# Optimization experiments

Measured on AMD Instinct MI355X. Metric: run time of the kernel, lower is better.

## Reference

```python
import jax, jax.numpy as jnp
import numpy as np

EPS = 1e-5

def conv(x, w, b=None, groups=1):
    kh, kw = w.shape[2], w.shape[3]
    y = jax.lax.conv_general_dilated(
        x, w, (1, 1), ((kh // 2, kh // 2), (kw // 2, kw // 2)),
        dimension_numbers=('NCHW', 'OIHW', 'NCHW'), feature_group_count=groups)
    if b is not None:
        y = y + b[None, :, None, None]
    return y

def layernorm_c(x, g, b):
    # LayerNorm over channel dim (module permutes to NHWC, norms last dim, permutes back)
    mu = jnp.mean(x, axis=1, keepdims=True)
    var = jnp.mean(jnp.square(x - mu), axis=1, keepdims=True)
    return (x - mu) * jax.lax.rsqrt(var + EPS) * g[None, :, None, None] + b[None, :, None, None]

def _bilinear(img, py, px):
    # img: (N,C,H,W); py,px: (N,H,W) float sampling coords; zero outside bounds
    H, W = img.shape[2], img.shape[3]
    y0 = jnp.floor(py); x0 = jnp.floor(px)
    wy1 = py - y0; wy0 = 1.0 - wy1
    wx1 = px - x0; wx0 = 1.0 - wx1

    def gather(yc, xc):
        valid = (yc >= 0) & (yc <= H - 1) & (xc >= 0) & (xc <= W - 1)
        yi = jnp.clip(yc, 0, H - 1).astype(jnp.int32)
        xi = jnp.clip(xc, 0, W - 1).astype(jnp.int32)
        v = jax.vmap(lambda im, yy, xx: im[:, yy, xx])(img, yi, xi)  # (N,C,H,W)
        return v * valid[:, None].astype(img.dtype)

    return (gather(y0, x0) * (wy0 * wx0)[:, None]
            + gather(y0, x0 + 1) * (wy0 * wx1)[:, None]
            + gather(y0 + 1, x0) * (wy1 * wx0)[:, None]
            + gather(y0 + 1, x0 + 1) * (wy1 * wx1)[:, None])

def deform_conv2d(x, offset, weight, mask):
    # torchvision-style modulated deformable conv, 3x3, pad=1, stride=1
    N, C, H, W = x.shape
    by, bx = jnp.meshgrid(jnp.arange(H, dtype=x.dtype), jnp.arange(W, dtype=x.dtype), indexing='ij')
    out = jnp.zeros((N, weight.shape[0], H, W), dtype=x.dtype)
    for i in range(3):
        for j in range(3):
            k = i * 3 + j
            py = by[None] + (i - 1) + offset[:, 2 * k]      # (N,H,W)
            px = bx[None] + (j - 1) + offset[:, 2 * k + 1]
            samp = _bilinear(x, py, px) * mask[:, k][:, None]  # (N,C,H,W)
            out = out + jnp.einsum('nchw,oc->nohw', samp, weight[:, :, i, j])
    return out

def _forward(input_flow, input_event,
             ln_flow_g, ln_flow_b, ln_event_g, ln_event_b,
             ff_w1, ff_b1, ff_w2, ff_b2,
             fo_w1, fo_b1, fo_w2, fo_b2,
             fm_w1, fm_b1, fm_w2, fm_b2,
             dc_weight,
             sf_w1, sf_b1, sf_w2, sf_b2, sf_w3, sf_b3, sf_w4, sf_b4,
             fl_w1, fl_b1, fl_w2, fl_b2):
    N, C, H, W = input_flow.shape
    flow_norm = layernorm_c(input_flow, ln_flow_g, ln_flow_b)
    event_norm = layernorm_c(input_event, ln_event_g, ln_event_b)
    x = conv(jax.nn.relu(conv(flow_norm, ff_w1, ff_b1)), ff_w2, ff_b2, groups=C)
    offset = conv(jax.nn.relu(conv(event_norm, fo_w1, fo_b1)), fo_w2, fo_b2)
    mask = jax.nn.sigmoid(conv(jax.nn.relu(conv(event_norm, fm_w1, fm_b1)), fm_w2, fm_b2))
    dc = deform_conv2d(x, offset, dc_weight, mask)
    x_fft = jnp.fft.rfft2(x)            # (N,C,H,W//2+1) complex
    dc_fft = jnp.fft.rfft2(dc)
    fft_cate = jnp.concatenate([dc_fft.real, dc_fft.imag], axis=1)  # (N,2C,H,Wf)
    h = conv(fft_cate, sf_w1, sf_b1)
    h = conv(h, sf_w2, sf_b2, groups=2 * C)
    h = jax.nn.relu(conv(h, sf_w3, sf_b3))
    sp_mask = jax.nn.sigmoid(conv(h, sf_w4, sf_b4))  # (N,C,H,Wf) real
    x_irfft = jnp.fft.irfft2(x_fft * sp_mask, s=(H, W))
    g = conv(x_irfft, fl_w1, fl_b1, groups=C)
    a, b = jnp.split(g, 2, axis=1)
    g = a * jax.nn.gelu(b, approximate=False)
    return conv(g, fl_w2, fl_b2) + input_flow

def setup_inputs() -> dict:
    key = jax.random.key(0)
    N, C, H, W = 8, 32, 256, 256
    ks = iter(jax.random.split(key, 64))
    rn = lambda shp, s=0.05: jax.random.normal(next(ks), shp, dtype=jnp.float32) * s
    d = {
        'input_flow': jax.random.normal(next(ks), (N, C, H, W), dtype=jnp.float32),
        'input_event': jax.random.normal(next(ks), (N, C, H, W), dtype=jnp.float32),
        'ln_flow_g': 1.0 + rn((C,), 0.1), 'ln_flow_b': rn((C,), 0.1),
        'ln_event_g': 1.0 + rn((C,), 0.1), 'ln_event_b': rn((C,), 0.1),
        'ff_w1': rn((C, C, 1, 1)), 'ff_b1': rn((C,)),
        'ff_w2': rn((C, 1, 3, 3)), 'ff_b2': rn((C,)),
        'fo_w1': rn((C, C, 1, 1)), 'fo_b1': rn((C,)),
        'fo_w2': rn((18, C, 3, 3)), 'fo_b2': rn((18,)),
        'fm_w1': rn((C, C, 1, 1)), 'fm_b1': rn((C,)),
        'fm_w2': rn((9, C, 3, 3)), 'fm_b2': rn((9,)),
        'dc_weight': rn((C, C, 3, 3)),
        'sf_w1': rn((2 * C, 2 * C, 1, 1)), 'sf_b1': rn((2 * C,)),
        'sf_w2': rn((2 * C, 1, 3, 3)), 'sf_b2': rn((2 * C,)),
        'sf_w3': rn((2 * C, 2 * C, 1, 1)), 'sf_b3': rn((2 * C,)),
        'sf_w4': rn((C, 2 * C, 1, 1)), 'sf_b4': rn((C,)),
        'fl_w1': rn((C, 1, 3, 3)), 'fl_b1': rn((C,)),
        'fl_w2': rn((C, C // 2, 1, 1)), 'fl_b2': rn((C,)),
    }
    return d

def reference(input_flow, input_event,
              ln_flow_g, ln_flow_b, ln_event_g, ln_event_b,
              ff_w1, ff_b1, ff_w2, ff_b2,
              fo_w1, fo_b1, fo_w2, fo_b2,
              fm_w1, fm_b1, fm_w2, fm_b2,
              dc_weight,
              sf_w1, sf_b1, sf_w2, sf_b2, sf_w3, sf_b3, sf_w4, sf_b4,
              fl_w1, fl_b1, fl_w2, fl_b2):
    return _forward(input_flow, input_event,
                    ln_flow_g, ln_flow_b, ln_event_g, ln_event_b,
                    ff_w1, ff_b1, ff_w2, ff_b2,
                    fo_w1, fo_b1, fo_w2, fo_b2,
                    fm_w1, fm_b1, fm_w2, fm_b2,
                    dc_weight,
                    sf_w1, sf_b1, sf_w2, sf_b2, sf_w3, sf_b3, sf_w4, sf_b4,
                    fl_w1, fl_b1, fl_w2, fl_b2)
```

## Files before the change

### kernel.cpp

```cpp
#include <hip/hip_runtime.h>
#include <cmath>

constexpr int kN = 8;
constexpr int kC = 32;
constexpr int kH = 256;
constexpr int kW = 256;
constexpr int kHW = kH * kW;
constexpr int kWF = 129;
constexpr int kHWF = kH * kWF;
constexpr float kPI = 3.14159265358979323846f;

__device__ __forceinline__ float sigmoidf_(float x) { return 1.f / (1.f + expf(-x)); }

__device__ __forceinline__ int xcd_swizzle(int bid, int nblk)
{
    int chunk = nblk >> 3;
    return (bid & 7) * chunk + (bid >> 3);
}

template <bool TWO>
__global__ __launch_bounds__(256) void lnmv_kernel(
    const float* __restrict__ in,
    const float* __restrict__ lng, const float* __restrict__ lnb,
    const float* __restrict__ w1, const float* __restrict__ b1, float* __restrict__ out1,
    const float* __restrict__ w2, const float* __restrict__ b2, float* __restrict__ out2)
{
    __shared__ __align__(16) float wl1[1024];
    __shared__ __align__(16) float wl2[TWO ? 1024 : 4];
    __shared__ float bl1[32], bl2[32], gl[32], bbl[32];
    int tid = threadIdx.x;
    for (int e = tid; e < 1024; e += 256) {
        wl1[e] = w1[e];
        if (TWO) wl2[e] = w2[e];
    }
    if (tid < 32) {
        bl1[tid] = b1[tid]; gl[tid] = lng[tid]; bbl[tid] = lnb[tid];
        if (TWO) bl2[tid] = b2[tid];
    }
    __syncthreads();

    int p = blockIdx.x * 256 + tid;
    int n = p >> 16;
    int rem = p & 65535;
    const float* base = in + (size_t)n * kC * kHW + rem;

    float v[32];
    float mu = 0.f;
#pragma unroll
    for (int c = 0; c < 32; ++c) { v[c] = base[(size_t)c * kHW]; mu += v[c]; }
    mu *= 0.03125f;
    float var = 0.f;
#pragma unroll
    for (int c = 0; c < 32; ++c) { float d = v[c] - mu; var += d * d; }
    var *= 0.03125f;
    float rs = rsqrtf(var + 1e-5f);
#pragma unroll
    for (int c = 0; c < 32; ++c) v[c] = (v[c] - mu) * rs * gl[c] + bbl[c];

    {
        float* o = out1 + (size_t)n * kC * kHW + rem;
#pragma unroll
        for (int oc = 0; oc < 32; ++oc) {
            const float4* wr = reinterpret_cast<const float4*>(wl1 + oc * 32);
            float acc = bl1[oc];
#pragma unroll
            for (int q = 0; q < 8; ++q) {
                float4 wv = wr[q];
                acc += wv.x * v[4*q] + wv.y * v[4*q+1] + wv.z * v[4*q+2] + wv.w * v[4*q+3];
            }
            o[(size_t)oc * kHW] = fmaxf(acc, 0.f);
        }
    }
    if (TWO) {
        float* o = out2 + (size_t)n * kC * kHW + rem;
#pragma unroll
        for (int oc = 0; oc < 32; ++oc) {
            const float4* wr = reinterpret_cast<const float4*>(wl2 + oc * 32);
            float acc = bl2[oc];
#pragma unroll
            for (int q = 0; q < 8; ++q) {
                float4 wv = wr[q];
                acc += wv.x * v[4*q] + wv.y * v[4*q+1] + wv.z * v[4*q+2] + wv.w * v[4*q+3];
            }
            o[(size_t)oc * kHW] = fmaxf(acc, 0.f);
        }
    }
}

__global__ __launch_bounds__(256) void dw3x3_kernel(
    const float* __restrict__ in, const float* __restrict__ w,
    const float* __restrict__ bias, float* __restrict__ out,
    int CH, int Hd, int Wd, int total)
{
    int sw = xcd_swizzle(blockIdx.x, gridDim.x);
    int idx = sw * 256 + threadIdx.x;
    if (idx >= total) return;
    int wx = idx % Wd;
    int rest = idx / Wd;
    int hy = rest % Hd;
    int pl = rest / Hd;
    int ch = pl % CH;

    const float* ip = in + (size_t)pl * Hd * Wd;
    const float* wp = w + ch * 9;
    float acc = bias[ch];
#pragma unroll
    for (int dy = -1; dy <= 1; ++dy) {
        int yy = hy + dy;
        if (yy < 0 || yy >= Hd) continue;
        const float* rp = ip + (size_t)yy * Wd;
#pragma unroll
        for (int dx = -1; dx <= 1; ++dx) {
            int xx = wx + dx;
            if (xx < 0 || xx >= Wd) continue;
            acc += rp[xx] * wp[(dy + 1) * 3 + (dx + 1)];
        }
    }
    out[idx] = acc;
}

template <int COUT, int COUTP, int ACT>
__global__ __launch_bounds__(256) void conv3x3_kernel(
    const float* __restrict__ in, const float* __restrict__ wg,
    const float* __restrict__ bias, float* __restrict__ out)
{
    __shared__ __align__(16) float wl[288 * COUTP];
    __shared__ float bl[COUT];
    int tid = threadIdx.x;
    for (int e = tid; e < 288 * COUTP; e += 256) {
        int oc = e % COUTP;
        int t = e / COUTP;
        wl[e] = (oc < COUT) ? wg[(oc * 32 + (t / 9)) * 9 + (t % 9)] : 0.f;
    }
    if (tid < COUT) bl[tid] = bias[tid];
    __syncthreads();

    int sw = xcd_swizzle(blockIdx.x, gridDim.x);
    int row = sw * 4 + (tid >> 6);
    int lane = tid & 63;
    int n = row >> 8;
    int h = row & 255;

    float acc[4][COUTP];
#pragma unroll
    for (int px = 0; px < 4; ++px)
#pragma unroll
        for (int oc = 0; oc < COUTP; ++oc) acc[px][oc] = (oc < COUT) ? bl[oc] : 0.f;

    const float* ib = in + (size_t)n * 32 * kHW;
    for (int ic = 0; ic < 32; ++ic) {
        const float* ipl = ib + (size_t)ic * kHW;
#pragma unroll
        for (int ky = 0; ky < 3; ++ky) {
            int yy = h + ky - 1;
            if (yy < 0 || yy > 255) continue;
            const float* rp = ipl + (size_t)yy * 256;
#pragma unroll
            for (int kx = 0; kx < 3; ++kx) {
                float val[4];
#pragma unroll
                for (int px = 0; px < 4; ++px) {
                    int xx = lane + px * 64 + kx - 1;
                    val[px] = (xx >= 0 && xx < 256) ? rp[xx] : 0.f;
                }
                const float4* wr = reinterpret_cast<const float4*>(wl + (ic * 9 + ky * 3 + kx) * COUTP);
#pragma unroll
                for (int q = 0; q < COUTP / 4; ++q) {
                    float4 wv = wr[q];
#pragma unroll
                    for (int px = 0; px < 4; ++px) {
                        acc[px][4*q+0] += val[px] * wv.x;
                        acc[px][4*q+1] += val[px] * wv.y;
                        acc[px][4*q+2] += val[px] * wv.z;
                        acc[px][4*q+3] += val[px] * wv.w;
                    }
                }
            }
        }
    }

    float* ob = out + (size_t)n * COUT * kHW + (size_t)h * 256;
#pragma unroll
    for (int oc = 0; oc < COUT; ++oc) {
#pragma unroll
        for (int px = 0; px < 4; ++px) {
            float r = acc[px][oc];
            if (ACT == 2) r = sigmoidf_(r);
            ob[(size_t)oc * kHW + lane + px * 64] = r;
        }
    }
}

__global__ __launch_bounds__(256) void deform_kernel(
    const float* __restrict__ x, const float* __restrict__ off,
    const float* __restrict__ msk, const float* __restrict__ wt,
    float* __restrict__ out)
{
    __shared__ __align__(16) float wl[9 * 32 * 32];
    int tid = threadIdx.x;
    for (int e = tid; e < 9216; e += 256) {
        int o = e & 31;
        int t = e >> 5;
        int c = t & 31;
        int k = t >> 5;
        wl[e] = wt[((size_t)(o * 32 + c)) * 9 + k];
    }
    __syncthreads();

    int sw = xcd_swizzle(blockIdx.x, gridDim.x);
    int row = sw * 4 + (tid >> 6);
    int lane = tid & 63;
    int n = row >> 8;
    int h = row & 255;
    int pixbase = h * 256 + lane;

    const float* offb = off + (size_t)n * 18 * kHW + pixbase;
    const float* mskb = msk + (size_t)n * 9 * kHW + pixbase;
    const float* xb = x + (size_t)n * 32 * kHW;

    float acc[4][32];
#pragma unroll
    for (int px = 0; px < 4; ++px)
#pragma unroll
        for (int oc = 0; oc < 32; ++oc) acc[px][oc] = 0.f;

    for (int k = 0; k < 9; ++k) {
        int ki = k / 3 - 1, kj = k % 3 - 1;
        int i00[4], i01[4], i10[4], i11[4];
        float w00[4], w01[4], w10[4], w11[4];
#pragma unroll
        for (int px = 0; px < 4; ++px) {
            int wx = lane + px * 64;
            float oy = offb[(size_t)(2 * k) * kHW + px * 64];
            float ox = offb[(size_t)(2 * k + 1) * kHW + px * 64];
            float m = mskb[(size_t)k * kHW + px * 64];
            float py = (float)(h + ki) + oy;
            float pxx = (float)(wx + kj) + ox;
            float y0f = floorf(py), x0f = floorf(pxx);
            float fy = py - y0f, fx = pxx - x0f;
            float vy0 = (y0f >= 0.f && y0f <= 255.f) ? 1.f : 0.f;
            float vy1 = (y0f >= -1.f && y0f <= 254.f) ? 1.f : 0.f;
            float vx0 = (x0f >= 0.f && x0f <= 255.f) ? 1.f : 0.f;
            float vx1 = (x0f >= -1.f && x0f <= 254.f) ? 1.f : 0.f;
            int y0 = min(max((int)y0f, 0), 255);
            int y1 = min(max((int)y0f + 1, 0), 255);
            int x0 = min(max((int)x0f, 0), 255);
            int x1 = min(max((int)x0f + 1, 0), 255);
            i00[px] = y0 * 256 + x0; i01[px] = y0 * 256 + x1;
            i10[px] = y1 * 256 + x0; i11[px] = y1 * 256 + x1;
            w00[px] = (1.f - fy) * (1.f - fx) * m * vy0 * vx0;
            w01[px] = (1.f - fy) * fx * m * vy0 * vx1;
            w10[px] = fy * (1.f - fx) * m * vy1 * vx0;
            w11[px] = fy * fx * m * vy1 * vx1;
        }
        for (int c = 0; c < 32; ++c) {
            const float* xp = xb + (size_t)c * kHW;
            float s[4];
#pragma unroll
            for (int px = 0; px < 4; ++px) {
                s[px] = w00[px] * xp[i00[px]] + w01[px] * xp[i01[px]] +
                        w10[px] * xp[i10[px]] + w11[px] * xp[i11[px]];
            }
            const float4* wr = reinterpret_cast<const float4*>(wl + (size_t)(k * 32 + c) * 32);
#pragma unroll
            for (int q = 0; q < 8; ++q) {
                float4 wv = wr[q];
#pragma unroll
                for (int px = 0; px < 4; ++px) {
                    acc[px][4*q+0] += s[px] * wv.x;
                    acc[px][4*q+1] += s[px] * wv.y;
                    acc[px][4*q+2] += s[px] * wv.z;
                    acc[px][4*q+3] += s[px] * wv.w;
                }
            }
        }
    }

    float* ob = out + (size_t)n * 32 * kHW + pixbase;
#pragma unroll
    for (int oc = 0; oc < 32; ++oc)
#pragma unroll
        for (int px = 0; px < 4; ++px)
            ob[(size_t)oc * kHW + px * 64] = acc[px][oc];
}

__device__ __forceinline__ void fft256_stages(float2* A, float2* Bb, const float2* tw,
                                              int lane, float sgn)
{
    float2* src = A;
    float2* dst = Bb;
#pragma unroll
    for (int s = 0; s < 4; ++s) {
        int m = 1 << (2 * s);
        int r = lane & (m - 1);
        int mc = lane - r;
        __syncthreads();
        float2 x0 = src[lane];
        float2 x1 = src[lane + 128];
        float2 x2 = src[lane + 64];
        float2 x3 = src[lane + 192];
        float2 wa = tw[mc];
        float2 wb = tw[mc + 64];
        float2 wc = tw[2 * mc];
        float way = wa.y * sgn, wby = wb.y * sgn, wcy = wc.y * sgn;
        float e1x = x0.x + x1.x, e1y = x0.y + x1.y;
        float d1x = x0.x - x1.x, d1y = x0.y - x1.y;
        float o1x = wa.x * d1x - way * d1y, o1y = wa.x * d1y + way * d1x;
        float e2x = x2.x + x3.x, e2y = x2.y + x3.y;
        float d2x = x2.x - x3.x, d2y = x2.y - x3.y;
        float o2x = wb.x * d2x - wby * d2y, o2y = wb.x * d2y + wby * d2x;
        int base = r + 4 * mc;
        float2 y0; y0.x = e1x + e2x; y0.y = e1y + e2y;
        float ex = e1x - e2x, ey = e1y - e2y;
        float2 y2; y2.x = wc.x * ex - wcy * ey; y2.y = wc.x * ey + wcy * ex;
        float2 y1; y1.x = o1x + o2x; y1.y = o1y + o2y;
        float ox = o1x - o2x, oy = o1y - o2y;
        float2 y3; y3.x = wc.x * ox - wcy * oy; y3.y = wc.x * oy + wcy * ox;
        dst[base] = y0;
        dst[base + m] = y1;
        dst[base + 2 * m] = y2;
        dst[base + 3 * m] = y3;
        float2* t = src; src = dst; dst = t;
    }
    __syncthreads();
}

__device__ __forceinline__ void make_tw(float2* tw, int tid)
{
    if (tid < 128) {
        float ang = -kPI * (float)tid / 128.f;
        float2 w; w.x = cosf(ang); w.y = sinf(ang);
        tw[tid] = w;
    }
}

__global__ __launch_bounds__(256) void fft_rows_r2c(const float* __restrict__ in,
                                                    float2* __restrict__ out)
{
    __shared__ float2 A[4][256];
    __shared__ float2 Bb[4][256];
    __shared__ float2 tw[128];
    int tid = threadIdx.x;
    int sub = tid >> 6, lane = tid & 63;
    make_tw(tw, tid);
    size_t row = (size_t)blockIdx.x * 4 + sub;
    const float* rp = in + row * 256;
#pragma unroll
    for (int r = 0; r < 4; ++r) {
        int i = lane + 64 * r;
        float2 a; a.x = rp[i]; a.y = 0.f;
        A[sub][i] = a;
    }
    fft256_stages(A[sub], Bb[sub], tw, lane, 1.f);
    float2* op = out + row * kWF;
    op[lane] = A[sub][lane];
    op[lane + 64] = A[sub][lane + 64];
    if (lane == 0) op[128] = A[sub][128];
}

__global__ __launch_bounds__(256) void fft_cols_c2c(float2* __restrict__ buf)
{
    __shared__ float2 A[4][256];
    __shared__ float2 Bb[4][256];
    __shared__ float2 tw[128];
    int tid = threadIdx.x;
    int sub = tid >> 6, lane = tid & 63;
    make_tw(tw, tid);
    int b = xcd_swizzle(blockIdx.x, gridDim.x);
    int p = b / 33;
    int col0 = (b % 33) * 4;
    int ncols = (col0 + 4 <= kWF) ? 4 : (kWF - col0);
    float2* base = buf + (size_t)p * kHWF + col0;
    for (int e = tid; e < 1024; e += 256) {
        int cc = e & 3, hh = e >> 2;
        if (cc < ncols) A[cc][hh] = base[(size_t)hh * kWF + cc];
    }
    fft256_stages(A[sub], Bb[sub], tw, lane, 1.f);
    for (int e = tid; e < 1024; e += 256) {
        int cc = e & 3, hh = e >> 2;
        if (cc < ncols) base[(size_t)hh * kWF + cc] = A[cc][hh];
    }
}

__global__ __launch_bounds__(256) void ifft_cols_mask(const float2* __restrict__ xf,
                                                      const float* __restrict__ spm,
                                                      float2* __restrict__ out)
{
    __shared__ float2 A[4][256];
    __shared__ float2 Bb[4][256];
    __shared__ float2 tw[128];
    int tid = threadIdx.x;
    int sub = tid >> 6, lane = tid & 63;
    make_tw(tw, tid);
    int b = xcd_swizzle(blockIdx.x, gridDim.x);
    int p = b / 33;
    int col0 = (b % 33) * 4;
    int ncols = (col0 + 4 <= kWF) ? 4 : (kWF - col0);
    const float2* xb = xf + (size_t)p * kHWF + col0;
    const float* mb = spm + (size_t)p * kHWF + col0;
    for (int e = tid; e < 1024; e += 256) {
        int cc = e & 3, hh = e >> 2;
        if (cc < ncols) {
            float2 a = xb[(size_t)hh * kWF + cc];
            float m = mb[(size_t)hh * kWF + cc];
            a.x *= m; a.y *= m;
            A[cc][hh] = a;
        }
    }
    fft256_stages(A[sub], Bb[sub], tw, lane, -1.f);
    float2* ob = out + (size_t)p * kHWF + col0;
    for (int e = tid; e < 1024; e += 256) {
        int cc = e & 3, hh = e >> 2;
        if (cc < ncols) ob[(size_t)hh * kWF + cc] = A[cc][hh];
    }
}

__global__ __launch_bounds__(256) void ifft_rows_c2r(const float2* __restrict__ in,
                                                     float* __restrict__ out)
{
    __shared__ float2 A[4][256];
    __shared__ float2 Bb[4][256];
    __shared__ float2 tw[128];
    int tid = threadIdx.x;
    int sub = tid >> 6, lane = tid & 63;
    make_tw(tw, tid);
    size_t row = (size_t)blockIdx.x * 4 + sub;
    const float2* ip = in + row * kWF;
#pragma unroll
    for (int r = 0; r < 4; ++r) {
        int k = lane + 64 * r;
        if (k <= 128) {
            A[sub][k] = ip[k];
        } else {
            float2 c = ip[256 - k];
            c.y = -c.y;
            A[sub][k] = c;
        }
    }
    fft256_stages(A[sub], Bb[sub], tw, lane, -1.f);
    float* op = out + row * 256;
#pragma unroll
    for (int r = 0; r < 4; ++r) {
        int k = lane + 64 * r;
        op[k] = A[sub][k].x * (1.f / 65536.f);
    }
}

template <int CIN, int COUT, int ACT, bool CPLX>
__global__ __launch_bounds__(256) void conv1x1_kernel(
    const void* __restrict__ inv, const float* __restrict__ wg,
    const float* __restrict__ bias, float* __restrict__ out)
{
    constexpr int PL = kHWF;
    __shared__ __align__(16) float wl[COUT * CIN];
    __shared__ float bl[COUT];
    int tid = threadIdx.x;
    for (int e = tid; e < COUT * CIN; e += 256) wl[e] = wg[e];
    if (tid < COUT) bl[tid] = bias[tid];
    __syncthreads();

    int p0 = blockIdx.x * 512 + tid;
    int p1 = p0 + 256;
    int n0 = p0 / PL, r0 = p0 % PL;
    int n1 = p1 / PL, r1 = p1 % PL;

    float v0[CIN], v1[CIN];
    if (CPLX) {
        const float2* in2 = (const float2*)inv;
#pragma unroll
        for (int c = 0; c < 32; ++c) {
            float2 a = in2[(size_t)(n0 * 32 + c) * PL + r0];
            float2 b = in2[(size_t)(n1 * 32 + c) * PL + r1];
            v0[c] = a.x; v0[32 + c] = a.y;
            v1[c] = b.x; v1[32 + c] = b.y;
        }
    } else {
        const float* inf_ = (const float*)inv;
#pragma unroll
        for (int c = 0; c < CIN; ++c) {
            v0[c] = inf_[(size_t)(n0 * CIN + c) * PL + r0];
            v1[c] = inf_[(size_t)(n1 * CIN + c) * PL + r1];
        }
    }

#pragma unroll
    for (int oc = 0; oc < COUT; ++oc) {
        const float4* wr = reinterpret_cast<const float4*>(wl + oc * CIN);
        float a0 = bl[oc], a1 = bl[oc];
#pragma unroll
        for (int q = 0; q < CIN / 4; ++q) {
            float4 wv = wr[q];
            a0 += wv.x * v0[4*q] + wv.y * v0[4*q+1] + wv.z * v0[4*q+2] + wv.w * v0[4*q+3];
            a1 += wv.x * v1[4*q] + wv.y * v1[4*q+1] + wv.z * v1[4*q+2] + wv.w * v1[4*q+3];
        }
        if (ACT == 1) { a0 = fmaxf(a0, 0.f); a1 = fmaxf(a1, 0.f); }
        if (ACT == 2) { a0 = sigmoidf_(a0); a1 = sigmoidf_(a1); }
        out[(size_t)(n0 * COUT + oc) * PL + r0] = a0;
        out[(size_t)(n1 * COUT + oc) * PL + r1] = a1;
    }
}

__global__ __launch_bounds__(256) void conv1x1_chain_kernel(
    const float* __restrict__ in, const float* __restrict__ w3,
    const float* __restrict__ b3, const float* __restrict__ w4,
    const float* __restrict__ b4, float* __restrict__ out)
{
    constexpr int PL = kHWF;
    __shared__ __align__(16) float wl3[64 * 64];
    __shared__ __align__(16) float wl4[32 * 64];
    __shared__ float bl3[64], bl4[32];
    int tid = threadIdx.x;
    for (int e = tid; e < 4096; e += 256) wl3[e] = w3[e];
    for (int e = tid; e < 2048; e += 256) wl4[e] = w4[e];
    if (tid < 64) bl3[tid] = b3[tid];
    if (tid < 32) bl4[tid] = b4[tid];
    __syncthreads();

    int p0 = blockIdx.x * 512 + tid;
    int p1 = p0 + 256;
    int n0 = p0 / PL, r0 = p0 % PL;
    int n1 = p1 / PL, r1 = p1 % PL;

    float v0[64], v1[64];
#pragma unroll
    for (int c = 0; c < 64; ++c) {
        v0[c] = in[(size_t)(n0 * 64 + c) * PL + r0];
        v1[c] = in[(size_t)(n1 * 64 + c) * PL + r1];
    }

    float t0[64], t1[64];
#pragma unroll
    for (int oc = 0; oc < 64; ++oc) {
        const float4* wr = reinterpret_cast<const float4*>(wl3 + oc * 64);
        float a0 = bl3[oc], a1 = bl3[oc];
#pragma unroll
        for (int q = 0; q < 16; ++q) {
            float4 wv = wr[q];
            a0 += wv.x * v0[4*q] + wv.y * v0[4*q+1] + wv.z * v0[4*q+2] + wv.w * v0[4*q+3];
            a1 += wv.x * v1[4*q] + wv.y * v1[4*q+1] + wv.z * v1[4*q+2] + wv.w * v1[4*q+3];
        }
        t0[oc] = fmaxf(a0, 0.f); t1[oc] = fmaxf(a1, 0.f);
    }

#pragma unroll
    for (int oc = 0; oc < 32; ++oc) {
        const float4* wr = reinterpret_cast<const float4*>(wl4 + oc * 64);
        float a0 = bl4[oc], a1 = bl4[oc];
#pragma unroll
        for (int q = 0; q < 16; ++q) {
            float4 wv = wr[q];
            a0 += wv.x * t0[4*q] + wv.y * t0[4*q+1] + wv.z * t0[4*q+2] + wv.w * t0[4*q+3];
            a1 += wv.x * t1[4*q] + wv.y * t1[4*q+1] + wv.z * t1[4*q+2] + wv.w * t1[4*q+3];
        }
        out[(size_t)(n0 * 32 + oc) * PL + r0] = sigmoidf_(a0);
        out[(size_t)(n1 * 32 + oc) * PL + r1] = sigmoidf_(a1);
    }
}

__global__ __launch_bounds__(256) void final_kernel(
    const float* __restrict__ g, const float* __restrict__ flow,
    const float* __restrict__ wg, const float* __restrict__ bias,
    float* __restrict__ out)
{
    __shared__ __align__(16) float wl[32 * 16];
    __shared__ float bl[32];
    int tid = threadIdx.x;
    for (int e = tid; e < 512; e += 256) wl[e] = wg[e];
    if (tid < 32) bl[tid] = bias[tid];
    __syncthreads();

    int p = blockIdx.x * 256 + tid;
    int n = p >> 16;
    int rem = p & 65535;
    const float* gb = g + (size_t)n * 32 * kHW + rem;

    float v[16];
#pragma unroll
    for (int c = 0; c < 16; ++c) {
        float a = gb[(size_t)c * kHW];
        float b = gb[(size_t)(16 + c) * kHW];
        float ge = 0.5f * b * (1.f + erff(b * 0.70710678118654752f));
        v[c] = a * ge;
    }

    const float* fb = flow + (size_t)n * 32 * kHW + rem;
    float* ob = out + (size_t)n * 32 * kHW + rem;
#pragma unroll
    for (int oc = 0; oc < 32; ++oc) {
        const float4* wr = reinterpret_cast<const float4*>(wl + oc * 16);
        float acc = bl[oc];
#pragma unroll
        for (int q = 0; q < 4; ++q) {
            float4 wv = wr[q];
            acc += wv.x * v[4*q] + wv.y * v[4*q+1] + wv.z * v[4*q+2] + wv.w * v[4*q+3];
        }
        ob[(size_t)oc * kHW] = acc + fb[(size_t)oc * kHW];
    }
}

extern "C" void kernel_launch(void* const* d_in, const int* in_sizes, int n_in,
                              void* d_out, int out_size, void* d_ws, size_t ws_size,
                              hipStream_t stream)
{
    (void)in_sizes; (void)n_in; (void)out_size; (void)ws_size;

    const float* input_flow  = (const float*)d_in[0];
    const float* input_event = (const float*)d_in[1];
    const float* ln_flow_g   = (const float*)d_in[2];
    const float* ln_flow_b   = (const float*)d_in[3];
    const float* ln_event_g  = (const float*)d_in[4];
    const float* ln_event_b  = (const float*)d_in[5];
    const float* ff_w1 = (const float*)d_in[6];
    const float* ff_b1 = (const float*)d_in[7];
    const float* ff_w2 = (const float*)d_in[8];
    const float* ff_b2 = (const float*)d_in[9];
    const float* fo_w1 = (const float*)d_in[10];
    const float* fo_b1 = (const float*)d_in[11];
    const float* fo_w2 = (const float*)d_in[12];
    const float* fo_b2 = (const float*)d_in[13];
    const float* fm_w1 = (const float*)d_in[14];
    const float* fm_b1 = (const float*)d_in[15];
    const float* fm_w2 = (const float*)d_in[16];
    const float* fm_b2 = (const float*)d_in[17];
    const float* dc_weight = (const float*)d_in[18];
    const float* sf_w1 = (const float*)d_in[19];
    const float* sf_b1 = (const float*)d_in[20];
    const float* sf_w2 = (const float*)d_in[21];
    const float* sf_b2 = (const float*)d_in[22];
    const float* sf_w3 = (const float*)d_in[23];
    const float* sf_b3 = (const float*)d_in[24];
    const float* sf_w4 = (const float*)d_in[25];
    const float* sf_b4 = (const float*)d_in[26];
    const float* fl_w1 = (const float*)d_in[27];
    const float* fl_b1 = (const float*)d_in[28];
    const float* fl_w2 = (const float*)d_in[29];
    const float* fl_b2 = (const float*)d_in[30];
    float* out = (float*)d_out;

    const size_t S = (size_t)16908288;
    float* A = (float*)d_ws;
    float* B = A + S;
    float* Cs = B + S;
    float* X = out;

    lnmv_kernel<false><<<2048, 256, 0, stream>>>(input_flow, ln_flow_g, ln_flow_b,
                                                 ff_w1, ff_b1, A,
                                                 nullptr, nullptr, nullptr);
    lnmv_kernel<true><<<2048, 256, 0, stream>>>(input_event, ln_event_g, ln_event_b,
                                                fo_w1, fo_b1, B,
                                                fm_w1, fm_b1, Cs);
    dw3x3_kernel<<<65536, 256, 0, stream>>>(A, ff_w2, ff_b2, X, 32, 256, 256, 16777216);
    conv3x3_kernel<18, 20, 0><<<512, 256, 0, stream>>>(B, fo_w2, fo_b2, A);
    conv3x3_kernel<9, 12, 2><<<512, 256, 0, stream>>>(Cs, fm_w2, fm_b2, B);
    deform_kernel<<<512, 256, 0, stream>>>(X, A, B, dc_weight, Cs);
    fft_rows_r2c<<<16384, 256, 0, stream>>>(X, (float2*)A);
    fft_cols_c2c<<<8448, 256, 0, stream>>>((float2*)A);
    fft_rows_r2c<<<16384, 256, 0, stream>>>(Cs, (float2*)B);
    fft_cols_c2c<<<8448, 256, 0, stream>>>((float2*)B);
    conv1x1_kernel<64, 64, 0, true><<<516, 256, 0, stream>>>((const void*)B, sf_w1, sf_b1, Cs);
    dw3x3_kernel<<<66048, 256, 0, stream>>>(Cs, sf_w2, sf_b2, B, 64, 256, 129, 16908288);
    conv1x1_chain_kernel<<<516, 256, 0, stream>>>(B, sf_w3, sf_b3, sf_w4, sf_b4, Cs);
    ifft_cols_mask<<<8448, 256, 0, stream>>>((const float2*)A, Cs, (float2*)B);
    ifft_rows_c2r<<<16384, 256, 0, stream>>>((const float2*)B, Cs);
    dw3x3_kernel<<<65536, 256, 0, stream>>>(Cs, fl_w1, fl_b1, A, 32, 256, 256, 16777216);
    final_kernel<<<2048, 256, 0, stream>>>(A, input_flow, fl_w2, fl_b2, out);
}
```

Measured before the change: 1.500 ms.

## Halve per-thread work in deform and 1x1 convs, widen column FFT tiles

The deformable conv kernel now handles 2 pixels per thread instead of 4 and launches twice the blocks. The 1x1 conv and chain kernels drop from two pixels per thread to one. Both changes cut register pressure and raise occupancy. The column FFT and inverse-FFT-with-mask kernels now process 16 columns per block in a padded (stride 17) shared layout instead of 4, so global loads along rows are wider and more coalesced. The cost is fewer blocks per FFT launch and more shared memory per block.

```diff
diff --git a/kernel.cpp b/kernel.cpp
--- a/kernel.cpp
+++ b/kernel.cpp
@@ -208,32 +208,33 @@
     __syncthreads();
 
     int sw = xcd_swizzle(blockIdx.x, gridDim.x);
-    int row = sw * 4 + (tid >> 6);
-    int lane = tid & 63;
+    int halfid = tid >> 7;
+    int l = tid & 127;
+    int row = sw * 2 + halfid;
     int n = row >> 8;
     int h = row & 255;
-    int pixbase = h * 256 + lane;
+    int pixbase = h * 256 + l;
 
     const float* offb = off + (size_t)n * 18 * kHW + pixbase;
     const float* mskb = msk + (size_t)n * 9 * kHW + pixbase;
     const float* xb = x + (size_t)n * 32 * kHW;
 
-    float acc[4][32];
-#pragma unroll
-    for (int px = 0; px < 4; ++px)
+    float acc[2][32];
+#pragma unroll
+    for (int px = 0; px < 2; ++px)
 #pragma unroll
         for (int oc = 0; oc < 32; ++oc) acc[px][oc] = 0.f;
 
     for (int k = 0; k < 9; ++k) {
         int ki = k / 3 - 1, kj = k % 3 - 1;
-        int i00[4], i01[4], i10[4], i11[4];
-        float w00[4], w01[4], w10[4], w11[4];
-#pragma unroll
-        for (int px = 0; px < 4; ++px) {
-            int wx = lane + px * 64;
-            float oy = offb[(size_t)(2 * k) * kHW + px * 64];
-            float ox = offb[(size_t)(2 * k + 1) * kHW + px * 64];
-            float m = mskb[(size_t)k * kHW + px * 64];
+        int i00[2], i01[2], i10[2], i11[2];
+        float w00[2], w01[2], w10[2], w11[2];
+#pragma unroll
+        for (int px = 0; px < 2; ++px) {
+            int wx = l + px * 128;
+            float oy = offb[(size_t)(2 * k) * kHW + px * 128];
+            float ox = offb[(size_t)(2 * k + 1) * kHW + px * 128];
+            float m = mskb[(size_t)k * kHW + px * 128];
             float py = (float)(h + ki) + oy;
             float pxx = (float)(wx + kj) + ox;
             float y0f = floorf(py), x0f = floorf(pxx);
@@ -253,11 +254,12 @@
             w10[px] = fy * (1.f - fx) * m * vy1 * vx0;
             w11[px] = fy * fx * m * vy1 * vx1;
         }
+#pragma unroll 2
         for (int c = 0; c < 32; ++c) {
             const float* xp = xb + (size_t)c * kHW;
-            float s[4];
-#pragma unroll
-            for (int px = 0; px < 4; ++px) {
+            float s[2];
+#pragma unroll
+            for (int px = 0; px < 2; ++px) {
                 s[px] = w00[px] * xp[i00[px]] + w01[px] * xp[i01[px]] +
                         w10[px] * xp[i10[px]] + w11[px] * xp[i11[px]];
             }
@@ -266,7 +268,7 @@
             for (int q = 0; q < 8; ++q) {
                 float4 wv = wr[q];
 #pragma unroll
-                for (int px = 0; px < 4; ++px) {
+                for (int px = 0; px < 2; ++px) {
                     acc[px][4*q+0] += s[px] * wv.x;
                     acc[px][4*q+1] += s[px] * wv.y;
                     acc[px][4*q+2] += s[px] * wv.z;
@@ -280,8 +282,8 @@
 #pragma unroll
     for (int oc = 0; oc < 32; ++oc)
 #pragma unroll
-        for (int px = 0; px < 4; ++px)
-            ob[(size_t)oc * kHW + px * 64] = acc[px][oc];
+        for (int px = 0; px < 2; ++px)
+            ob[(size_t)oc * kHW + px * 128] = acc[px][oc];
 }
 
 __device__ __forceinline__ void fft256_stages(float2* A, float2* Bb, const float2* tw,
@@ -325,6 +327,51 @@
     __syncthreads();
 }
 
+__device__ __forceinline__ void fft256_stages16(float2* A, float2* Bb, const float2* tw,
+                                                int t, int c, float sgn)
+{
+    float2* src = A;
+    float2* dst = Bb;
+#pragma unroll
+    for (int s = 0; s < 4; ++s) {
+        int m = 1 << (2 * s);
+        __syncthreads();
+#pragma unroll
+        for (int b = 0; b < 4; ++b) {
+            int q = t + (b << 4);
+            int r = q & (m - 1);
+            int mc = q - r;
+            float2 x0 = src[q * 17 + c];
+            float2 x1 = src[(q + 128) * 17 + c];
+            float2 x2 = src[(q + 64) * 17 + c];
+            float2 x3 = src[(q + 192) * 17 + c];
+            float2 wa = tw[mc];
+            float2 wb = tw[mc + 64];
+            float2 wc = tw[2 * mc];
+            float way = wa.y * sgn, wby = wb.y * sgn, wcy = wc.y * sgn;
+            float e1x = x0.x + x1.x, e1y = x0.y + x1.y;
+            float d1x = x0.x - x1.x, d1y = x0.y - x1.y;
+            float o1x = wa.x * d1x - way * d1y, o1y = wa.x * d1y + way * d1x;
+            float e2x = x2.x + x3.x, e2y = x2.y + x3.y;
+            float d2x = x2.x - x3.x, d2y = x2.y - x3.y;
+            float o2x = wb.x * d2x - wby * d2y, o2y = wb.x * d2y + wby * d2x;
+            int base = r + 4 * mc;
+            float2 y0; y0.x = e1x + e2x; y0.y = e1y + e2y;
+            float ex = e1x - e2x, ey = e1y - e2y;
+            float2 y2; y2.x = wc.x * ex - wcy * ey; y2.y = wc.x * ey + wcy * ex;
+            float2 y1; y1.x = o1x + o2x; y1.y = o1y + o2y;
+            float ox = o1x - o2x, oy = o1y - o2y;
+            float2 y3; y3.x = wc.x * ox - wcy * oy; y3.y = wc.x * oy + wcy * ox;
+            dst[base * 17 + c] = y0;
+            dst[(base + m) * 17 + c] = y1;
+            dst[(base + 2 * m) * 17 + c] = y2;
+            dst[(base + 3 * m) * 17 + c] = y3;
+        }
+        float2* tp = src; src = dst; dst = tp;
+    }
+    __syncthreads();
+}
+
 __device__ __forceinline__ void make_tw(float2* tw, int tid)
 {
     if (tid < 128) {
@@ -358,60 +405,62 @@
     if (lane == 0) op[128] = A[sub][128];
 }
 
-__global__ __launch_bounds__(256) void fft_cols_c2c(float2* __restrict__ buf)
-{
-    __shared__ float2 A[4][256];
-    __shared__ float2 Bb[4][256];
+__global__ __launch_bounds__(256) void fft_cols16(float2* __restrict__ buf)
+{
+    __shared__ float2 A[256 * 17];
+    __shared__ float2 Bb[256 * 17];
     __shared__ float2 tw[128];
     int tid = threadIdx.x;
-    int sub = tid >> 6, lane = tid & 63;
     make_tw(tw, tid);
     int b = xcd_swizzle(blockIdx.x, gridDim.x);
-    int p = b / 33;
-    int col0 = (b % 33) * 4;
-    int ncols = (col0 + 4 <= kWF) ? 4 : (kWF - col0);
+    int p = b / 9;
+    int grp = b % 9;
+    int col0 = grp * 16;
+    int ncols = (col0 + 16 <= kWF) ? 16 : (kWF - col0);
     float2* base = buf + (size_t)p * kHWF + col0;
-    for (int e = tid; e < 1024; e += 256) {
-        int cc = e & 3, hh = e >> 2;
-        if (cc < ncols) A[cc][hh] = base[(size_t)hh * kWF + cc];
-    }
-    fft256_stages(A[sub], Bb[sub], tw, lane, 1.f);
-    for (int e = tid; e < 1024; e += 256) {
-        int cc = e & 3, hh = e >> 2;
-        if (cc < ncols) base[(size_t)hh * kWF + cc] = A[cc][hh];
-    }
-}
-
-__global__ __launch_bounds__(256) void ifft_cols_mask(const float2* __restrict__ xf,
-                                                      const float* __restrict__ spm,
-                                                      float2* __restrict__ out)
-{
-    __shared__ float2 A[4][256];
-    __shared__ float2 Bb[4][256];
+    for (int e = tid; e < 4096; e += 256) {
+        int pp = e >> 4, cc = e & 15;
+        if (cc < ncols) A[pp * 17 + cc] = base[(size_t)pp * kWF + cc];
+    }
+    int c = tid & 15, t = tid >> 4;
+    fft256_stages16(A, Bb, tw, t, c, 1.f);
+    for (int e = tid; e < 4096; e += 256) {
+        int pp = e >> 4, cc = e & 15;
+        if (cc < ncols) base[(size_t)pp * kWF + cc] = A[pp * 17 + cc];
+    }
+}
+
+__global__ __launch_bounds__(256) void ifft_cols_mask16(const float2* __restrict__ xf,
+                                                        const float* __restrict__ spm,
+                                                        float2* __restrict__ out)
+{
+    __shared__ float2 A[256 * 17];
+    __shared__ float2 Bb[256 * 17];
     __shared__ float2 tw[128];
     int tid = threadIdx.x;
-    int sub = tid >> 6, lane = tid & 63;
     make_tw(tw, tid);
     int b = xcd_swizzle(blockIdx.x, gridDim.x);
-    int p = b / 33;
-    int col0 = (b % 33) * 4;
-    int ncols = (col0 + 4 <= kWF) ? 4 : (kWF - col0);
+    int p = b / 9;
+    int grp = b % 9;
+    int col0 = grp * 16;
+    int ncols = (col0 + 16 <= kWF) ? 16 : (kWF - col0);
     const float2* xb = xf + (size_t)p * kHWF + col0;
     const float* mb = spm + (size_t)p * kHWF + col0;
-    for (int e = tid; e < 1024; e += 256) {
-        int cc = e & 3, hh = e >> 2;
+    for (int e = tid; e < 4096; e += 256) {
+        int pp = e >> 4, cc = e & 15;
         if (cc < ncols) {
-            float2 a = xb[(size_t)hh * kWF + cc];
-            float m = mb[(size_t)hh * kWF + cc];
+            float2 a = xb[(size_t)pp * kWF + cc];
+            float m = mb[(size_t)pp * kWF + cc];
             a.x *= m; a.y *= m;
-            A[cc][hh] = a;
-        }
-    }
-    fft256_stages(A[sub], Bb[sub], tw, lane, -1.f);
+            A[pp * 17 + cc] = a;
+        }
+    }
+    int c = tid & 15, t = tid >> 4;
+    fft256_stages16(A, Bb, tw, t, c, -1.f);
     float2* ob = out + (size_t)p * kHWF + col0;
-    for (int e = tid; e < 1024; e += 256) {
-        int cc = e & 3, hh = e >> 2;
-        if (cc < ncols) ob[(size_t)hh * kWF + cc] = A[cc][hh];
+    for (int e = tid; e < 4096; e += 256) {
+        int pp = e >> 4, cc = e & 15;
+        if (cc < ncols) ob[(size_t)pp * kWF + cc] = A[pp * 17 + cc];
     }
 }
 
@@ -459,44 +508,37 @@
     if (tid < COUT) bl[tid] = bias[tid];
     __syncthreads();
 
-    int p0 = blockIdx.x * 512 + tid;
-    int p1 = p0 + 256;
+    int p0 = blockIdx.x * 256 + tid;
     int n0 = p0 / PL, r0 = p0 % PL;
-    int n1 = p1 / PL, r1 = p1 % PL;
-
-    float v0[CIN], v1[CIN];
+
+    float v0[CIN];
     if (CPLX) {
         const float2* in2 = (const float2*)inv;
 #pragma unroll
         for (int c = 0; c < 32; ++c) {
             float2 a = in2[(size_t)(n0 * 32 + c) * PL + r0];
-            float2 b = in2[(size_t)(n1 * 32 + c) * PL + r1];
             v0[c] = a.x; v0[32 + c] = a.y;
-            v1[c] = b.x; v1[32 + c] = b.y;
         }
     } else {
         const float* inf_ = (const float*)inv;
 #pragma unroll
         for (int c = 0; c < CIN; ++c) {
             v0[c] = inf_[(size_t)(n0 * CIN + c) * PL + r0];
-            v1[c] = inf_[(size_t)(n1 * CIN + c) * PL + r1];
         }
     }
 
 #pragma unroll
     for (int oc = 0; oc < COUT; ++oc) {
         const float4* wr = reinterpret_cast<const float4*>(wl + oc * CIN);
-        float a0 = bl[oc], a1 = bl[oc];
+        float a0 = bl[oc];
 #pragma unroll
         for (int q = 0; q < CIN / 4; ++q) {
             float4 wv = wr[q];
             a0 += wv.x * v0[4*q] + wv.y * v0[4*q+1] + wv.z * v0[4*q+2] + wv.w * v0[4*q+3];
-            a1 += wv.x * v1[4*q] + wv.y * v1[4*q+1] + wv.z * v1[4*q+2] + wv.w * v1[4*q+3];
-        }
-        if (ACT == 1) { a0 = fmaxf(a0, 0.f); a1 = fmaxf(a1, 0.f); }
-        if (ACT == 2) { a0 = sigmoidf_(a0); a1 = sigmoidf_(a1); }
+        }
+        if (ACT == 1) a0 = fmaxf(a0, 0.f);
+        if (ACT == 2) a0 = sigmoidf_(a0);
         out[(size_t)(n0 * COUT + oc) * PL + r0] = a0;
-        out[(size_t)(n1 * COUT + oc) * PL + r1] = a1;
     }
 }
 
@@ -516,44 +558,36 @@
     if (tid < 32) bl4[tid] = b4[tid];
     __syncthreads();
 
-    int p0 = blockIdx.x * 512 + tid;
-    int p1 = p0 + 256;
+    int p0 = blockIdx.x * 256 + tid;
     int n0 = p0 / PL, r0 = p0 % PL;
-    int n1 = p1 / PL, r1 = p1 % PL;
-
-    float v0[64], v1[64];
-#pragma unroll
-    for (int c = 0; c < 64; ++c) {
-        v0[c] = in[(size_t)(n0 * 64 + c) * PL + r0];
-        v1[c] = in[(size_t)(n1 * 64 + c) * PL + r1];
-    }
-
-    float t0[64], t1[64];
+
+    float v0[64];
+#pragma unroll
+    for (int c = 0; c < 64; ++c) v0[c] = in[(size_t)(n0 * 64 + c) * PL + r0];
+
+    float t0[64];
 #pragma unroll
     for (int oc = 0; oc < 64; ++oc) {
         const float4* wr = reinterpret_cast<const float4*>(wl3 + oc * 64);
-        float a0 = bl3[oc], a1 = bl3[oc];
+        float a0 = bl3[oc];
 #pragma unroll
         for (int q = 0; q < 16; ++q) {
             float4 wv = wr[q];
             a0 += wv.x * v0[4*q] + wv.y * v0[4*q+1] + wv.z * v0[4*q+2] + wv.w * v0[4*q+3];
-            a1 += wv.x * v1[4*q] + wv.y * v1[4*q+1] + wv.z * v1[4*q+2] + wv.w * v1[4*q+3];
-        }
-        t0[oc] = fmaxf(a0, 0.f); t1[oc] = fmaxf(a1, 0.f);
+        }
+        t0[oc] = fmaxf(a0, 0.f);
     }
 
 #pragma unroll
     for (int oc = 0; oc < 32; ++oc) {
         const float4* wr = reinterpret_cast<const float4*>(wl4 + oc * 64);
-        float a0 = bl4[oc], a1 = bl4[oc];
+        float a0 = bl4[oc];
 #pragma unroll
         for (int q = 0; q < 16; ++q) {
             float4 wv = wr[q];
             a0 += wv.x * t0[4*q] + wv.y * t0[4*q+1] + wv.z * t0[4*q+2] + wv.w * t0[4*q+3];
-            a1 += wv.x * t1[4*q] + wv.y * t1[4*q+1] + wv.z * t1[4*q+2] + wv.w * t1[4*q+3];
         }
         out[(size_t)(n0 * 32 + oc) * PL + r0] = sigmoidf_(a0);
-        out[(size_t)(n1 * 32 + oc) * PL + r1] = sigmoidf_(a1);
     }
 }
 
@@ -652,15 +686,15 @@
     dw3x3_kernel<<<65536, 256, 0, stream>>>(A, ff_w2, ff_b2, X, 32, 256, 256, 16777216);
     conv3x3_kernel<18, 20, 0><<<512, 256, 0, stream>>>(B, fo_w2, fo_b2, A);
     conv3x3_kernel<9, 12, 2><<<512, 256, 0, stream>>>(Cs, fm_w2, fm_b2, B);
-    deform_kernel<<<512, 256, 0, stream>>>(X, A, B, dc_weight, Cs);
+    deform_kernel<<<1024, 256, 0, stream>>>(X, A, B, dc_weight, Cs);
     fft_rows_r2c<<<16384, 256, 0, stream>>>(X, (float2*)A);
-    fft_cols_c2c<<<8448, 256, 0, stream>>>((float2*)A);
+    fft_cols16<<<2304, 256, 0, stream>>>((float2*)A);
     fft_rows_r2c<<<16384, 256, 0, stream>>>(Cs, (float2*)B);
-    fft_cols_c2c<<<8448, 256, 0, stream>>>((float2*)B);
-    conv1x1_kernel<64, 64, 0, true><<<516, 256, 0, stream>>>((const void*)B, sf_w1, sf_b1, Cs);
+    fft_cols16<<<2304, 256, 0, stream>>>((float2*)B);
+    conv1x1_kernel<64, 64, 0, true><<<1032, 256, 0, stream>>>((const void*)B, sf_w1, sf_b1, Cs);
     dw3x3_kernel<<<66048, 256, 0, stream>>>(Cs, sf_w2, sf_b2, B, 64, 256, 129, 16908288);
-    conv1x1_chain_kernel<<<516, 256, 0, stream>>>(B, sf_w3, sf_b3, sf_w4, sf_b4, Cs);
-    ifft_cols_mask<<<8448, 256, 0, stream>>>((const float2*)A, Cs, (float2*)B);
+    conv1x1_chain_kernel<<<1032, 256, 0, stream>>>(B, sf_w3, sf_b3, sf_w4, sf_b4, Cs);
+    ifft_cols_mask16<<<2304, 256, 0, stream>>>((const float2*)A, Cs, (float2*)B);
     ifft_rows_c2r<<<16384, 256, 0, stream>>>((const float2*)B, Cs);
     dw3x3_kernel<<<65536, 256, 0, stream>>>(Cs, fl_w1, fl_b1, A, 32, 256, 256, 16777216);
     final_kernel<<<2048, 256, 0, stream>>>(A, input_flow, fl_w2, fl_b2, out);
```

Result: faster. 1.447 ms (-3.5%).
